# Kernel optimization log

Hardware: AMD Instinct MI355X
Metric: run time of the kernel (lower is better)

## Reference

```python
import jax, jax.numpy as jnp
import numpy as np

N = 100000   # nodes
E = 1600000  # edges
H = 128      # num_features == hidden_size
C = 64       # num_classes
BN_EPS = 1e-5


def setup_inputs() -> dict:
    key = jax.random.key(0)
    ks = jax.random.split(key, 11)
    return {
        "x": jax.random.normal(ks[0], (N, H), jnp.float32),
        "edge_index": jax.random.randint(ks[1], (2, E), 0, N, dtype=jnp.int32),
        "edge_attr": jax.random.normal(ks[2], (E,), jnp.float32),
        "conv_w": jax.random.normal(ks[3], (2, 3, H, H), jnp.float32) / np.sqrt(H).astype(np.float32),
        "conv_b": jax.random.normal(ks[4], (2, 3, H), jnp.float32) * 0.1,
        "bn_g": jax.random.uniform(ks[5], (2, 3, H), jnp.float32, 0.5, 1.5),
        "bn_b": jax.random.normal(ks[6], (2, 3, H), jnp.float32) * 0.1,
        "bn_m": jax.random.normal(ks[7], (2, 3, H), jnp.float32) * 0.1,
        "bn_v": jax.random.uniform(ks[8], (2, 3, H), jnp.float32, 0.5, 1.5),
        "fc_w": jax.random.normal(ks[9], (H, C), jnp.float32) / np.sqrt(H).astype(np.float32),
        "fc_b": jax.random.normal(ks[10], (C,), jnp.float32) * 0.1,
    }


def _gin_conv(h, edge_index, w, b, g, beta, m, v):
    # GIN: out = MLP((1+eps)*x + sum_{j in N(i)} x_j), eps=0 (PyG default)
    src, dst = edge_index[0], edge_index[1]
    agg = jax.ops.segment_sum(h[src], dst, num_segments=N)  # [N,H] scatter-add
    h = h + agg
    for i in range(3):  # Linear -> BatchNorm1d (eval stats) -> ReLU
        h = h @ w[i] + b[i]
        h = (h - m[i]) * jax.lax.rsqrt(v[i] + BN_EPS) * g[i] + beta[i]
        h = jax.nn.relu(h)
    return h


def reference(x, edge_index, edge_attr, conv_w, conv_b, bn_g, bn_b, bn_m, bn_v, fc_w, fc_b):
    # edge_attr is ignored by default PyG GINConv (no edge weighting in GIN)
    h = jax.nn.relu(_gin_conv(x, edge_index, conv_w[0], conv_b[0], bn_g[0], bn_b[0], bn_m[0], bn_v[0]))
    h = jax.nn.relu(_gin_conv(h, edge_index, conv_w[1], conv_b[1], bn_g[1], bn_b[1], bn_m[1], bn_v[1]))
    # dropout is identity in eval mode
    logits = h @ fc_w + fc_b  # [N,C]
    return jax.nn.log_softmax(logits, axis=1)
```

## Files before the change

### kernel.cpp

```cpp
#include <hip/hip_runtime.h>

#define NN 100000
#define NE 1600000
#define HF 128
#define NC 64
#define AP 136
#define NB 391
#define BSH 8
#define BMASK 255
#define BCAP 4608

typedef __bf16 bf16x8 __attribute__((ext_vector_type(8)));
typedef float  f32x4  __attribute__((ext_vector_type(4)));
typedef float  f32x2  __attribute__((ext_vector_type(2)));
typedef unsigned short us8 __attribute__((ext_vector_type(8)));
typedef unsigned int u32x4 __attribute__((ext_vector_type(4)));

__device__ __forceinline__ unsigned short f2b(float x) {
  unsigned int u = __float_as_uint(x);
  u += 0x7FFFu + ((u >> 16) & 1u);
  return (unsigned short)(u >> 16);
}
__device__ __forceinline__ float b2f(unsigned short b) {
  return __uint_as_float(((unsigned int)b) << 16);
}

__device__ __forceinline__ void addrow(f32x2 acc[4], u32x4 w) {
  #pragma unroll
  for (int i = 0; i < 4; i++) {
    f32x2 p;
    p.x = __uint_as_float(w[i] << 16);
    p.y = __uint_as_float(w[i] & 0xFFFF0000u);
    acc[i] += p;
  }
}

__global__ __launch_bounds__(512) void prologue_bin(const float* __restrict__ x,
                                                    unsigned short* __restrict__ xb,
                                                    const float* __restrict__ conv_w,
                                                    const float* __restrict__ conv_b,
                                                    const float* __restrict__ bn_g,
                                                    const float* __restrict__ bn_b,
                                                    const float* __restrict__ bn_m,
                                                    const float* __restrict__ bn_v,
                                                    const float* __restrict__ fc_w,
                                                    unsigned short* __restrict__ wt,
                                                    unsigned short* __restrict__ wtf,
                                                    float* __restrict__ sarr,
                                                    float* __restrict__ tarr,
                                                    int* __restrict__ gcur,
                                                    const int* __restrict__ src,
                                                    const int* __restrict__ dst,
                                                    unsigned int* __restrict__ binned) {
  __shared__ int hist[NB];
  int t = threadIdx.x;
  int idx = blockIdx.x * 512 + t;
  {
    size_t i = (size_t)idx * 8;
    float4 a = *(const float4*)(x + i);
    float4 b = *(const float4*)(x + i + 4);
    us8 v = { f2b(a.x), f2b(a.y), f2b(a.z), f2b(a.w),
              f2b(b.x), f2b(b.y), f2b(b.z), f2b(b.w) };
    *(us8*)(xb + i) = v;
  }
  if (idx < 3 * HF) {
    int k = idx >> 7, jj = idx & 127;
    xb[(size_t)k * (NN + 1) * HF + (size_t)NN * HF + jj] = 0;
  }
  if (idx < 6 * HF * HF) {
    int j  = idx & 7;
    int m  = (idx >> 3) & 15;
    int q  = (idx >> 7) & 3;
    int nt = (idx >> 9) & 7;
    int k0 = (idx >> 12) & 3;
    int ls = idx >> 14;
    int k = k0 * 32 + q * 8 + j;
    int n = nt * 16 + m;
    wt[idx] = f2b(conv_w[(ls * HF + k) * HF + n]);
  }
  if (idx < HF * NC) {
    int j  = idx & 7;
    int m  = (idx >> 3) & 15;
    int q  = (idx >> 7) & 3;
    int nt = (idx >> 9) & 3;
    int k0 = idx >> 11;
    int k = k0 * 32 + q * 8 + j;
    int c = nt * 16 + m;
    wtf[idx] = f2b(fc_w[k * NC + c]);
  }
  if (idx < 6 * HF) {
    float s = bn_g[idx] * rsqrtf(bn_v[idx] + 1e-5f);
    sarr[idx] = s;
    tarr[idx] = (conv_b[idx] - bn_m[idx]) * s + bn_b[idx];
  }
  if (blockIdx.x < NB) {
    if (t < NB) hist[t] = 0;
    __syncthreads();
    int base = blockIdx.x * 4096;
    int sv[8], dv[8];
    #pragma unroll
    for (int j = 0; j < 8; j++) {
      int e = base + j * 512 + t;
      bool ok = e < NE;
      dv[j] = ok ? dst[e] : -1;
      sv[j] = ok ? src[e] : 0;
      if (ok) atomicAdd(&hist[dv[j] >> BSH], 1);
    }
    __syncthreads();
    if (t < NB) {
      int c = hist[t];
      if (c) hist[t] = t * BCAP + atomicAdd(&gcur[t], c);
    }
    __syncthreads();
    #pragma unroll
    for (int j = 0; j < 8; j++) {
      if (dv[j] >= 0) {
        int b = dv[j] >> BSH;
        int p = atomicAdd(&hist[b], 1);
        binned[p] = (unsigned int)sv[j] | ((unsigned int)(dv[j] & BMASK) << 17);
      }
    }
  }
}

__global__ __launch_bounds__(512) void build_csr(const unsigned int* __restrict__ binned,
                                                 const int* __restrict__ gcur,
                                                 int* __restrict__ offs,
                                                 int* __restrict__ deg,
                                                 int* __restrict__ csr) {
  __shared__ int ncnt[256];
  __shared__ int sm[256];
  int t = threadIdx.x;
  int b = blockIdx.x;
  int beg = b * BCAP;
  int cntb = gcur[b];
  if (t < 256) ncnt[t] = 0;
  __syncthreads();
  for (int e = beg + t; e < beg + cntb; e += 512) atomicAdd(&ncnt[binned[e] >> 17], 1);
  __syncthreads();
  int s = 0;
  if (t < 256) { s = ncnt[t]; sm[t] = s; }
  __syncthreads();
  for (int off = 1; off < 256; off <<= 1) {
    int u = (t < 256 && t >= off) ? sm[t - off] : 0;
    __syncthreads();
    if (t < 256) sm[t] += u;
    __syncthreads();
  }
  if (t < 256) {
    int ex = sm[t] - s + beg;
    int node = (b << BSH) + t;
    if (node < NN) { offs[node] = ex; deg[node] = s; }
    ncnt[t] = ex;
  }
  __syncthreads();
  for (int e = beg + t; e < beg + cntb; e += 512) {
    unsigned int u = binned[e];
    int p = atomicAdd(&ncnt[u >> 17], 1);
    csr[p] = (int)(u & 0x1FFFFu);
  }
}

__global__ __launch_bounds__(256) void aggregate(const unsigned short* __restrict__ h,
                                                 const int* __restrict__ offs,
                                                 const int* __restrict__ deg,
                                                 const int* __restrict__ csr,
                                                 unsigned short* __restrict__ out) {
  int wave = threadIdx.x >> 6;
  int lane = threadIdx.x & 63;
  int node = blockIdx.x * 4 + wave;
  int g  = lane >> 4;
  int sl = lane & 15;
  int beg = offs[node];
  int dg  = deg[node];
  int n  = dg + 1;
  int nf = n < 64 ? n : 64;

  int myidx = NN;
  if (lane < nf) myidx = (lane == dg) ? node : csr[beg + lane];

  f32x2 acc[4];
  #pragma unroll
  for (int i = 0; i < 4; i++) acc[i] = (f32x2){0.f, 0.f};

  int K = (nf + 3) >> 2;
  int j = 0;
  for (; j + 3 < K; j += 4) {
    int s0 = __shfl(myidx, (j + 0) * 4 + g);
    int s1 = __shfl(myidx, (j + 1) * 4 + g);
    int s2 = __shfl(myidx, (j + 2) * 4 + g);
    int s3 = __shfl(myidx, (j + 3) * 4 + g);
    u32x4 v0 = *(const u32x4*)(h + (size_t)s0 * HF + sl * 8);
    u32x4 v1 = *(const u32x4*)(h + (size_t)s1 * HF + sl * 8);
    u32x4 v2 = *(const u32x4*)(h + (size_t)s2 * HF + sl * 8);
    u32x4 v3 = *(const u32x4*)(h + (size_t)s3 * HF + sl * 8);
    addrow(acc, v0);
    addrow(acc, v1);
    addrow(acc, v2);
    addrow(acc, v3);
  }
  for (; j + 1 < K; j += 2) {
    int s0 = __shfl(myidx, (j + 0) * 4 + g);
    int s1 = __shfl(myidx, (j + 1) * 4 + g);
    u32x4 v0 = *(const u32x4*)(h + (size_t)s0 * HF + sl * 8);
    u32x4 v1 = *(const u32x4*)(h + (size_t)s1 * HF + sl * 8);
    addrow(acc, v0);
    addrow(acc, v1);
  }
  if (j < K) {
    int s0 = __shfl(myidx, j * 4 + g);
    u32x4 v0 = *(const u32x4*)(h + (size_t)s0 * HF + sl * 8);
    addrow(acc, v0);
  }

  if (dg >= 64) {
    for (int e = beg + 64 + g; e < beg + dg; e += 4) {
      int s = csr[e];
      u32x4 v = *(const u32x4*)(h + (size_t)s * HF + sl * 8);
      addrow(acc, v);
    }
    if (g == 0) {
      u32x4 v = *(const u32x4*)(h + (size_t)node * HF + sl * 8);
      addrow(acc, v);
    }
  }

  #pragma unroll
  for (int i = 0; i < 4; i++) {
    acc[i].x += __shfl_xor(acc[i].x, 16, 64);
    acc[i].y += __shfl_xor(acc[i].y, 16, 64);
    acc[i].x += __shfl_xor(acc[i].x, 32, 64);
    acc[i].y += __shfl_xor(acc[i].y, 32, 64);
  }
  if (g == 0) {
    us8 r;
    #pragma unroll
    for (int i = 0; i < 4; i++) {
      r[2 * i]     = f2b(acc[i].x);
      r[2 * i + 1] = f2b(acc[i].y);
    }
    *(us8*)(out + (size_t)node * HF + sl * 8) = r;
  }
}

__device__ __forceinline__ void mlp3_body(const unsigned short* __restrict__ in,
                                          unsigned short* Ab,
                                          const unsigned short* __restrict__ wt,
                                          const float* __restrict__ sarr,
                                          const float* __restrict__ tarr,
                                          int layer, int row0, int wave, int lane,
                                          bf16x8 af[4]) {
  int m = lane & 15, q = lane >> 4;
  int node = row0 + wave * 16 + m;
  int nclamp = (node < NN) ? node : 0;
  #pragma unroll
  for (int k0 = 0; k0 < 4; k0++)
    af[k0] = *(const bf16x8*)(in + (size_t)nclamp * HF + k0 * 32 + q * 8);

  const unsigned short* wbase = wt + layer * 3 * 16384;
  #pragma unroll
  for (int sub = 0; sub < 3; sub++) {
    const unsigned short* wsub = wbase + sub * 16384;
    f32x4 acc[8];
    #pragma unroll
    for (int nt = 0; nt < 8; nt++) {
      acc[nt] = (f32x4){0.f, 0.f, 0.f, 0.f};
      #pragma unroll
      for (int k0 = 0; k0 < 4; k0++) {
        bf16x8 bf = *(const bf16x8*)(wsub + ((k0 * 8 + nt) * 64 + lane) * 8);
        acc[nt] = __builtin_amdgcn_mfma_f32_16x16x32_bf16(af[k0], bf, acc[nt], 0, 0, 0);
      }
    }
    const float* sp = sarr + (layer * 3 + sub) * HF;
    const float* tp = tarr + (layer * 3 + sub) * HF;
    #pragma unroll
    for (int nt = 0; nt < 8; nt++) {
      int c = nt * 16 + m;
      float sc = sp[c], sh = tp[c];
      #pragma unroll
      for (int i = 0; i < 4; i++) {
        int r = wave * 16 + q * 4 + i;
        float y = fmaxf(acc[nt][i] * sc + sh, 0.f);
        Ab[r * AP + c] = f2b(y);
      }
    }
    #pragma unroll
    for (int k0 = 0; k0 < 4; k0++)
      af[k0] = *(const bf16x8*)&Ab[(wave * 16 + m) * AP + k0 * 32 + q * 8];
  }
}

__global__ __launch_bounds__(256) void mlp3(const unsigned short* __restrict__ in,
                                            unsigned short* __restrict__ out,
                                            const unsigned short* __restrict__ wt,
                                            const float* __restrict__ sarr,
                                            const float* __restrict__ tarr) {
  __shared__ unsigned short Ab[64 * AP];
  int t = threadIdx.x;
  int lane = t & 63, wave = t >> 6;
  int row0 = blockIdx.x * 64;
  bf16x8 af[4];
  mlp3_body(in, Ab, wt, sarr, tarr, 0, row0, wave, lane, af);

  for (int it = 0; it < 4; it++) {
    int idx = it * 64 + lane;
    int r = wave * 16 + (idx >> 4);
    int c = (idx & 15) << 3;
    int gr = row0 + r;
    if (gr < NN) *(us8*)(out + (size_t)gr * HF + c) = *(const us8*)&Ab[r * AP + c];
  }
}

__global__ __launch_bounds__(256) void mlp3fc(const unsigned short* __restrict__ in,
                                              float* __restrict__ out,
                                              const unsigned short* __restrict__ wt,
                                              const float* __restrict__ sarr,
                                              const float* __restrict__ tarr,
                                              const unsigned short* __restrict__ wtf,
                                              const float* __restrict__ fc_b) {
  __shared__ unsigned short Ab[64 * AP];
  int t = threadIdx.x;
  int lane = t & 63, wave = t >> 6;
  int row0 = blockIdx.x * 64;
  int m = lane & 15, q = lane >> 4;
  bf16x8 af[4];
  mlp3_body(in, Ab, wt, sarr, tarr, 1, row0, wave, lane, af);

  f32x4 acc[4];
  #pragma unroll
  for (int nt = 0; nt < 4; nt++) {
    acc[nt] = (f32x4){0.f, 0.f, 0.f, 0.f};
    #pragma unroll
    for (int k0 = 0; k0 < 4; k0++) {
      bf16x8 bf = *(const bf16x8*)(wtf + ((k0 * 4 + nt) * 64 + lane) * 8);
      acc[nt] = __builtin_amdgcn_mfma_f32_16x16x32_bf16(af[k0], bf, acc[nt], 0, 0, 0);
    }
  }
  float v[4][4];
  #pragma unroll
  for (int nt = 0; nt < 4; nt++) {
    float b = fc_b[nt * 16 + m];
    #pragma unroll
    for (int i = 0; i < 4; i++) v[nt][i] = acc[nt][i] + b;
  }
  float mx[4], sum[4];
  #pragma unroll
  for (int i = 0; i < 4; i++) {
    mx[i] = fmaxf(fmaxf(v[0][i], v[1][i]), fmaxf(v[2][i], v[3][i]));
    mx[i] = fmaxf(mx[i], __shfl_xor(mx[i], 1, 64));
    mx[i] = fmaxf(mx[i], __shfl_xor(mx[i], 2, 64));
    mx[i] = fmaxf(mx[i], __shfl_xor(mx[i], 4, 64));
    mx[i] = fmaxf(mx[i], __shfl_xor(mx[i], 8, 64));
    sum[i] = __expf(v[0][i] - mx[i]) + __expf(v[1][i] - mx[i])
           + __expf(v[2][i] - mx[i]) + __expf(v[3][i] - mx[i]);
    sum[i] += __shfl_xor(sum[i], 1, 64);
    sum[i] += __shfl_xor(sum[i], 2, 64);
    sum[i] += __shfl_xor(sum[i], 4, 64);
    sum[i] += __shfl_xor(sum[i], 8, 64);
    sum[i] = __logf(sum[i]) + mx[i];
  }
  #pragma unroll
  for (int i = 0; i < 4; i++) {
    int gr = row0 + wave * 16 + q * 4 + i;
    if (gr < NN) {
      #pragma unroll
      for (int nt = 0; nt < 4; nt++)
        out[(size_t)gr * NC + nt * 16 + m] = v[nt][i] - sum[i];
    }
  }
}

extern "C" void kernel_launch(void* const* d_in, const int* in_sizes, int n_in,
                              void* d_out, int out_size, void* d_ws, size_t ws_size,
                              hipStream_t stream) {
  const float* x      = (const float*)d_in[0];
  const int*   ei     = (const int*)d_in[1];
  const float* conv_w = (const float*)d_in[3];
  const float* conv_b = (const float*)d_in[4];
  const float* bn_g   = (const float*)d_in[5];
  const float* bn_b   = (const float*)d_in[6];
  const float* bn_m   = (const float*)d_in[7];
  const float* bn_v   = (const float*)d_in[8];
  const float* fc_w   = (const float*)d_in[9];
  const float* fc_b   = (const float*)d_in[10];
  float* out = (float*)d_out;

  const int* srcI = ei;
  const int* dstI = ei + NE;

  unsigned short* Xb   = (unsigned short*)d_ws;
  unsigned short* Abuf = Xb + (size_t)(NN + 1) * HF;
  unsigned short* Bbuf = Abuf + (size_t)(NN + 1) * HF;
  int* gcur   = (int*)(Bbuf + (size_t)(NN + 1) * HF);
  int* offs   = gcur + 512;
  int* deg    = offs + 100004;
  unsigned int* binned = (unsigned int*)(deg + 100004);
  int* csr    = (int*)(binned + (size_t)NB * BCAP);
  unsigned short* wt  = (unsigned short*)(csr + (size_t)NB * BCAP);
  unsigned short* wtf = wt + 6 * HF * HF;
  float* sarr = (float*)(wtf + HF * NC);
  float* tarr = sarr + 6 * HF;

  hipMemsetAsync(gcur, 0, sizeof(int) * NB, stream);
  prologue_bin<<<3125, 512, 0, stream>>>(x, Xb, conv_w, conv_b, bn_g, bn_b, bn_m, bn_v,
                                         fc_w, wt, wtf, sarr, tarr, gcur,
                                         srcI, dstI, binned);
  build_csr<<<NB, 512, 0, stream>>>(binned, gcur, offs, deg, csr);

  aggregate<<<NN / 4, 256, 0, stream>>>(Xb, offs, deg, csr, Abuf);
  mlp3<<<(NN + 63) / 64, 256, 0, stream>>>(Abuf, Bbuf, wt, sarr, tarr);
  aggregate<<<NN / 4, 256, 0, stream>>>(Bbuf, offs, deg, csr, Abuf);
  mlp3fc<<<(NN + 63) / 64, 256, 0, stream>>>(Abuf, out, wt, sarr, tarr, wtf, fc_b);
}
```

Before: 327.7 us.

## Spread edge binning over more blocks with per-bucket sub-segment counters

Measured after the change: 341.9 us. 4.3% more time.

```diff
diff --git a/kernel.cpp b/kernel.cpp
--- a/kernel.cpp
+++ b/kernel.cpp
@@ -8,7 +8,9 @@
 #define NB 391
 #define BSH 8
 #define BMASK 255
-#define BCAP 4608
+#define BCAP 5120
+#define SEG 640
+#define NBB 1564
 
 typedef __bf16 bf16x8 __attribute__((ext_vector_type(8)));
 typedef float  f32x4  __attribute__((ext_vector_type(4)));
@@ -20,9 +22,6 @@
   unsigned int u = __float_as_uint(x);
   u += 0x7FFFu + ((u >> 16) & 1u);
   return (unsigned short)(u >> 16);
-}
-__device__ __forceinline__ float b2f(unsigned short b) {
-  return __uint_as_float(((unsigned int)b) << 16);
 }
 
 __device__ __forceinline__ void addrow(f32x2 acc[4], u32x4 w) {
@@ -93,13 +92,14 @@
     sarr[idx] = s;
     tarr[idx] = (conv_b[idx] - bn_m[idx]) * s + bn_b[idx];
   }
-  if (blockIdx.x < NB) {
+  if (blockIdx.x < NBB) {
     if (t < NB) hist[t] = 0;
     __syncthreads();
-    int base = blockIdx.x * 4096;
-    int sv[8], dv[8];
-    #pragma unroll
-    for (int j = 0; j < 8; j++) {
+    int base = blockIdx.x * 1024;
+    int rep  = blockIdx.x & 7;
+    int sv[2], dv[2];
+    #pragma unroll
+    for (int j = 0; j < 2; j++) {
       int e = base + j * 512 + t;
       bool ok = e < NE;
       dv[j] = ok ? dst[e] : -1;
@@ -109,11 +109,11 @@
     __syncthreads();
     if (t < NB) {
       int c = hist[t];
-      if (c) hist[t] = t * BCAP + atomicAdd(&gcur[t], c);
+      if (c) hist[t] = t * BCAP + rep * SEG + atomicAdd(&gcur[t * 8 + rep], c);
     }
     __syncthreads();
     #pragma unroll
-    for (int j = 0; j < 8; j++) {
+    for (int j = 0; j < 2; j++) {
       if (dv[j] >= 0) {
         int b = dv[j] >> BSH;
         int p = atomicAdd(&hist[b], 1);
@@ -130,13 +130,18 @@
                                                  int* __restrict__ csr) {
   __shared__ int ncnt[256];
   __shared__ int sm[256];
+  __shared__ int segc[8];
   int t = threadIdx.x;
   int b = blockIdx.x;
-  int beg = b * BCAP;
-  int cntb = gcur[b];
+  if (t < 8) segc[t] = gcur[b * 8 + t];
   if (t < 256) ncnt[t] = 0;
   __syncthreads();
-  for (int e = beg + t; e < beg + cntb; e += 512) atomicAdd(&ncnt[binned[e] >> 17], 1);
+  #pragma unroll
+  for (int r = 0; r < 8; r++) {
+    int sbeg = b * BCAP + r * SEG;
+    int c8 = segc[r];
+    for (int e = sbeg + t; e < sbeg + c8; e += 512) atomicAdd(&ncnt[binned[e] >> 17], 1);
+  }
   __syncthreads();
   int s = 0;
   if (t < 256) { s = ncnt[t]; sm[t] = s; }
@@ -148,16 +153,21 @@
     __syncthreads();
   }
   if (t < 256) {
-    int ex = sm[t] - s + beg;
+    int ex = sm[t] - s + b * BCAP;
     int node = (b << BSH) + t;
     if (node < NN) { offs[node] = ex; deg[node] = s; }
     ncnt[t] = ex;
   }
   __syncthreads();
-  for (int e = beg + t; e < beg + cntb; e += 512) {
-    unsigned int u = binned[e];
-    int p = atomicAdd(&ncnt[u >> 17], 1);
-    csr[p] = (int)(u & 0x1FFFFu);
+  #pragma unroll
+  for (int r = 0; r < 8; r++) {
+    int sbeg = b * BCAP + r * SEG;
+    int c8 = segc[r];
+    for (int e = sbeg + t; e < sbeg + c8; e += 512) {
+      unsigned int u = binned[e];
+      int p = atomicAdd(&ncnt[u >> 17], 1);
+      csr[p] = (int)(u & 0x1FFFFu);
+    }
   }
 }
 
@@ -169,6 +179,7 @@
   int wave = threadIdx.x >> 6;
   int lane = threadIdx.x & 63;
   int node = blockIdx.x * 4 + wave;
+  if (node >= NN) return;
   int g  = lane >> 4;
   int sl = lane & 15;
   int beg = offs[node];
@@ -392,7 +403,7 @@
   unsigned short* Abuf = Xb + (size_t)(NN + 1) * HF;
   unsigned short* Bbuf = Abuf + (size_t)(NN + 1) * HF;
   int* gcur   = (int*)(Bbuf + (size_t)(NN + 1) * HF);
-  int* offs   = gcur + 512;
+  int* offs   = gcur + 4096;
   int* deg    = offs + 100004;
   unsigned int* binned = (unsigned int*)(deg + 100004);
   int* csr    = (int*)(binned + (size_t)NB * BCAP);
@@ -401,7 +412,7 @@
   float* sarr = (float*)(wtf + HF * NC);
   float* tarr = sarr + 6 * HF;
 
-  hipMemsetAsync(gcur, 0, sizeof(int) * NB, stream);
+  hipMemsetAsync(gcur, 0, sizeof(int) * 4096, stream);
   prologue_bin<<<3125, 512, 0, stream>>>(x, Xb, conv_w, conv_b, bn_g, bn_b, bn_m, bn_v,
                                          fc_w, wt, wtf, sarr, tarr, gcur,
                                          srcI, dstI, binned);
```
